# Performance work log

Hardware: AMD Instinct MI355X
Metric: run time of the kernel (lower is better)

## Reference

```python
import jax, jax.numpy as jnp
import numpy as np

DIM = 256
BATCH = 131072


def setup_inputs() -> dict:
    key = jax.random.key(0)
    kx, kl, ku = jax.random.split(key, 3)
    x = jax.random.normal(kx, (BATCH, DIM), dtype=jnp.float32)
    # l: unit lower-triangular (eye + strict lower random), as in __init__
    l = jnp.eye(DIM, dtype=jnp.float32) + jnp.tril(
        jax.random.normal(kl, (DIM, DIM), dtype=jnp.float32), -1)
    # u: unit upper-triangular (eye + strict upper random)
    u = jnp.eye(DIM, dtype=jnp.float32) + jnp.triu(
        jax.random.normal(ku, (DIM, DIM), dtype=jnp.float32), 1)
    # p: fixed random permutation matrix (buffer, not trained)
    perm = np.random.RandomState(0).permutation(DIM)
    p = jnp.zeros((DIM, DIM), dtype=jnp.float32).at[
        np.arange(DIM), perm].set(1.0)
    return {"x": x, "p": p, "l": l, "u": u}


def reference(x, p, l, u):
    # forward (reverse=False): w = p @ l @ u ; y = (w @ x.T).T = x @ w.T
    w = p @ l @ u                      # [dim, dim]
    y = x @ w.T                        # [batch, dim]
    # log|det(w)| = log|det(u)| since p is a permutation (|det|=1) and l is
    # unit-triangular; u is upper-triangular so det(u) = prod(diag(u)).
    log_det = jnp.sum(jnp.log(jnp.abs(jnp.diag(u))))
    return (y, log_det)
```

## Files before the change

### kernel.cpp

```cpp
#include <hip/hip_runtime.h>

#define DIM 256
#define BATCH 131072
#define BM 64

typedef __attribute__((ext_vector_type(8))) short s16x8;
typedef __attribute__((ext_vector_type(8))) unsigned short u16x8;
typedef __attribute__((ext_vector_type(4))) float f32x4;

static __device__ __forceinline__ unsigned short f2bf(float f) {
    unsigned int u = __builtin_bit_cast(unsigned int, f);
    u = (u + 0x7FFFu + ((u >> 16) & 1u)) >> 16;
    return (unsigned short)u;
}

static __device__ __forceinline__ s16x8 cvt8(const float4 a, const float4 b) {
    return (s16x8){ (short)f2bf(a.x), (short)f2bf(a.y), (short)f2bf(a.z), (short)f2bf(a.w),
                    (short)f2bf(b.x), (short)f2bf(b.y), (short)f2bf(b.z), (short)f2bf(b.w) };
}

__global__ void lu_perm(const float* __restrict__ l, const float* __restrict__ u,
                        const float* __restrict__ p, unsigned short* __restrict__ wpk) {
    __shared__ float sL[DIM];
    __shared__ int dest;
    const int i = blockIdx.x, j = threadIdx.x;
    sL[j] = l[i * DIM + j];
    if (p[j * DIM + i] != 0.0f) dest = j;
    __syncthreads();
    float s0 = 0.f, s1 = 0.f, s2 = 0.f, s3 = 0.f;
    #pragma unroll 4
    for (int k = 0; k < DIM; k += 4) {
        s0 = fmaf(sL[k + 0], u[(k + 0) * DIM + j], s0);
        s1 = fmaf(sL[k + 1], u[(k + 1) * DIM + j], s1);
        s2 = fmaf(sL[k + 2], u[(k + 2) * DIM + j], s2);
        s3 = fmaf(sL[k + 3], u[(k + 3) * DIM + j], s3);
    }
    const int d = dest;
    const int idx = ((d >> 4) * 8 + (j >> 5)) * 512 + (((j >> 3) & 3) * 16 + (d & 15)) * 8 + (j & 7);
    wpk[idx] = f2bf((s0 + s1) + (s2 + s3));
}

__global__ void logdet_kernel(const float* __restrict__ u, float* __restrict__ out) {
    const int i = threadIdx.x;
    float v = logf(fabsf(u[i * DIM + i]));
    #pragma unroll
    for (int o = 32; o; o >>= 1) v += __shfl_down(v, o, 64);
    __shared__ float partial[4];
    if ((i & 63) == 0) partial[i >> 6] = v;
    __syncthreads();
    if (i == 0) out[0] = (partial[0] + partial[1]) + (partial[2] + partial[3]);
}

__global__ __launch_bounds__(256, 3) void gemm_xwT(const float* __restrict__ x,
                                                   const unsigned short* __restrict__ wpk,
                                                   float* __restrict__ y) {
    __shared__ unsigned short sA[4 * 8 * 512];

    const int t    = threadIdx.x;
    const int lane = t & 63;
    const int wc   = t >> 6;
    const int lr   = lane & 15;
    const int lg   = lane >> 4;
    const long row0 = (long)blockIdx.x * BM;

    const int sr  = t >> 2;
    const int kq  = t & 3;
    const int r15 = sr & 15;
    const int mb  = t >> 6;
    const float* asrc = x + (row0 + sr) * DIM + kq * 8;
    const int lpx = (kq * 16 + r15) ^ (kq << 1);
    #pragma unroll
    for (int q = 0; q < 8; ++q) {
        const float4 v0 = *(const float4*)(asrc + q * 32);
        const float4 v1 = *(const float4*)(asrc + q * 32 + 4);
        *(s16x8*)&sA[(mb * 8 + q) * 512 + (lpx ^ q) * 8] = cvt8(v0, v1);
    }

    const unsigned short* bbase = wpk + wc * 4 * 8 * 512 + lane * 8;
    const int lx = lane ^ ((lane >> 4) << 1);

    f32x4 acc[4][4];
    #pragma unroll
    for (int mi = 0; mi < 4; mi++)
        #pragma unroll
        for (int n = 0; n < 4; n++) acc[mi][n] = (f32x4){0.f, 0.f, 0.f, 0.f};

    s16x8 bf[2][4];
    #pragma unroll
    for (int n = 0; n < 4; n++)
        bf[0][n] = __builtin_bit_cast(s16x8, *(const u16x8*)(bbase + n * 8 * 512));

    __syncthreads();

    #pragma unroll
    for (int ks = 0; ks < 8; ++ks) {
        if (ks < 7) {
            #pragma unroll
            for (int n = 0; n < 4; n++)
                bf[(ks + 1) & 1][n] = __builtin_bit_cast(s16x8,
                    *(const u16x8*)(bbase + (n * 8 + ks + 1) * 512));
        }
        s16x8 af[4];
        #pragma unroll
        for (int mi = 0; mi < 4; mi++)
            af[mi] = *(const s16x8*)&sA[(mi * 8 + ks) * 512 + (lx ^ ks) * 8];
        #pragma unroll
        for (int mi = 0; mi < 4; mi++)
            #pragma unroll
            for (int n = 0; n < 4; n++)
                acc[mi][n] = __builtin_amdgcn_mfma_f32_16x16x32_bf16(
                    af[mi], bf[ks & 1][n], acc[mi][n], 0, 0, 0);
    }

    __syncthreads();

    float* ep = (float*)sA + wc * 1088;
    #pragma unroll
    for (int mi = 0; mi < 4; ++mi) {
        #pragma unroll
        for (int n = 0; n < 4; n++)
            #pragma unroll
            for (int j = 0; j < 4; j++)
                ep[(lg * 4 + j) * 68 + n * 16 + lr] = acc[mi][n][j];
        #pragma unroll
        for (int it = 0; it < 4; ++it) {
            const int row = it * 4 + lg;
            const float4 v = *(const float4*)&ep[row * 68 + lr * 4];
            *(float4*)&y[(row0 + mi * 16 + row) * DIM + wc * 64 + lr * 4] = v;
        }
    }
}

extern "C" void kernel_launch(void* const* d_in, const int* in_sizes, int n_in,
                              void* d_out, int out_size, void* d_ws, size_t ws_size,
                              hipStream_t stream) {
    const float* x = (const float*)d_in[0];
    const float* p = (const float*)d_in[1];
    const float* l = (const float*)d_in[2];
    const float* u = (const float*)d_in[3];
    float* out = (float*)d_out;

    unsigned short* wpk = (unsigned short*)d_ws;

    lu_perm<<<DIM, DIM, 0, stream>>>(l, u, p, wpk);
    logdet_kernel<<<1, DIM, 0, stream>>>(u, out + (size_t)BATCH * DIM);
    gemm_xwT<<<BATCH / BM, 256, 0, stream>>>(x, wpk, out);
}
```

Measured before the change: 62.94 us.

## Make GEMM persistent over several row tiles with double-buffered x prefetch

The GEMM kernel now uses 512-thread blocks that each walk 8 consecutive 32-row tiles. The next tile's x rows are prefetched into registers while the current tile is converted to bf16 in double-buffered LDS and multiplied. The LDS-staged epilogue is dropped in favour of direct scalar stores of the accumulators, and W fragments are reloaded from global memory for every tile. The intent is to hide global load latency and cut launch and tail overhead. The cost is less coalesced output stores (16 floats per row segment instead of float4) and repeated W reads.

```diff
diff --git a/kernel.cpp b/kernel.cpp
--- a/kernel.cpp
+++ b/kernel.cpp
@@ -2,7 +2,9 @@
 
 #define DIM 256
 #define BATCH 131072
-#define BM 64
+#define BM 32
+#define TPB 8
+#define NBLK (BATCH / (BM * TPB))
 
 typedef __attribute__((ext_vector_type(8))) short s16x8;
 typedef __attribute__((ext_vector_type(8))) unsigned short u16x8;
@@ -51,83 +53,90 @@
     if (i == 0) out[0] = (partial[0] + partial[1]) + (partial[2] + partial[3]);
 }
 
-__global__ __launch_bounds__(256, 3) void gemm_xwT(const float* __restrict__ x,
+__global__ __launch_bounds__(512, 4) void gemm_xwT(const float* __restrict__ x,
                                                    const unsigned short* __restrict__ wpk,
                                                    float* __restrict__ y) {
-    __shared__ unsigned short sA[4 * 8 * 512];
+    __shared__ unsigned short sA[2][16 * 512];
 
     const int t    = threadIdx.x;
     const int lane = t & 63;
-    const int wc   = t >> 6;
+    const int wid  = t >> 6;
     const int lr   = lane & 15;
     const int lg   = lane >> 4;
-    const long row0 = (long)blockIdx.x * BM;
+    const long base = (long)blockIdx.x * (BM * TPB);
 
-    const int sr  = t >> 2;
-    const int kq  = t & 3;
-    const int r15 = sr & 15;
-    const int mb  = t >> 6;
-    const float* asrc = x + (row0 + sr) * DIM + kq * 8;
-    const int lpx = (kq * 16 + r15) ^ (kq << 1);
+    const int srow = t >> 4;
+    const int kq2  = t & 15;
+    const int sks  = kq2 >> 1;
+    const int shs  = kq2 & 1;
+    const int smi  = srow >> 4;
+    const int slr  = srow & 15;
+    const float* asrc = x + (base + srow) * DIM + kq2 * 16;
+
+    const unsigned short* bbase = wpk + (wid * 2) * (8 * 512) + lane * 8;
+
+    float4 pf[2][4];
     #pragma unroll
-    for (int q = 0; q < 8; ++q) {
-        const float4 v0 = *(const float4*)(asrc + q * 32);
-        const float4 v1 = *(const float4*)(asrc + q * 32 + 4);
-        *(s16x8*)&sA[(mb * 8 + q) * 512 + (lpx ^ q) * 8] = cvt8(v0, v1);
-    }
-
-    const unsigned short* bbase = wpk + wc * 4 * 8 * 512 + lane * 8;
-    const int lx = lane ^ ((lane >> 4) << 1);
-
-    f32x4 acc[4][4];
-    #pragma unroll
-    for (int mi = 0; mi < 4; mi++)
-        #pragma unroll
-        for (int n = 0; n < 4; n++) acc[mi][n] = (f32x4){0.f, 0.f, 0.f, 0.f};
-
-    s16x8 bf[2][4];
-    #pragma unroll
-    for (int n = 0; n < 4; n++)
-        bf[0][n] = __builtin_bit_cast(s16x8, *(const u16x8*)(bbase + n * 8 * 512));
-
-    __syncthreads();
+    for (int q = 0; q < 4; q++) pf[0][q] = *(const float4*)(asrc + q * 4);
 
     #pragma unroll
-    for (int ks = 0; ks < 8; ++ks) {
-        if (ks < 7) {
+    for (int tt = 0; tt < TPB; tt++) {
+        const int cur = tt & 1;
+        if (tt + 1 < TPB) {
+            const float* nsrc = asrc + (long)(tt + 1) * BM * DIM;
             #pragma unroll
-            for (int n = 0; n < 4; n++)
-                bf[(ks + 1) & 1][n] = __builtin_bit_cast(s16x8,
-                    *(const u16x8*)(bbase + (n * 8 + ks + 1) * 512));
+            for (int q = 0; q < 4; q++)
+                pf[(tt + 1) & 1][q] = *(const float4*)(nsrc + q * 4);
         }
-        s16x8 af[4];
         #pragma unroll
-        for (int mi = 0; mi < 4; mi++)
-            af[mi] = *(const s16x8*)&sA[(mi * 8 + ks) * 512 + (lx ^ ks) * 8];
+        for (int h = 0; h < 2; h++) {
+            const int lgw = shs * 2 + h;
+            const int lperm = (lgw * 16 + slr) ^ (sks << 1);
+            *(s16x8*)&sA[cur][(sks * 2 + smi) * 512 + lperm * 8] =
+                cvt8(pf[cur][2 * h], pf[cur][2 * h + 1]);
+        }
+        asm volatile("s_waitcnt lgkmcnt(0)" ::: "memory");
+        __builtin_amdgcn_s_barrier();
+
+        f32x4 acc[2][2];
         #pragma unroll
-        for (int mi = 0; mi < 4; mi++)
+        for (int mi = 0; mi < 2; mi++)
             #pragma unroll
-            for (int n = 0; n < 4; n++)
-                acc[mi][n] = __builtin_amdgcn_mfma_f32_16x16x32_bf16(
-                    af[mi], bf[ks & 1][n], acc[mi][n], 0, 0, 0);
-    }
+            for (int n = 0; n < 2; n++) acc[mi][n] = (f32x4){0.f, 0.f, 0.f, 0.f};
 
-    __syncthreads();
+        s16x8 bf[2][2];
+        #pragma unroll
+        for (int n = 0; n < 2; n++)
+            bf[0][n] = __builtin_bit_cast(s16x8, *(const u16x8*)(bbase + (n * 8) * 512));
 
-    float* ep = (float*)sA + wc * 1088;
-    #pragma unroll
-    for (int mi = 0; mi < 4; ++mi) {
         #pragma unroll
-        for (int n = 0; n < 4; n++)
+        for (int ks = 0; ks < 8; ++ks) {
+            if (ks < 7) {
+                #pragma unroll
+                for (int n = 0; n < 2; n++)
+                    bf[(ks + 1) & 1][n] = __builtin_bit_cast(s16x8,
+                        *(const u16x8*)(bbase + (n * 8 + ks + 1) * 512));
+            }
+            s16x8 af[2];
             #pragma unroll
-            for (int j = 0; j < 4; j++)
-                ep[(lg * 4 + j) * 68 + n * 16 + lr] = acc[mi][n][j];
+            for (int mi = 0; mi < 2; mi++)
+                af[mi] = *(const s16x8*)&sA[cur][(ks * 2 + mi) * 512 + (lane ^ (ks << 1)) * 8];
+            #pragma unroll
+            for (int mi = 0; mi < 2; mi++)
+                #pragma unroll
+                for (int n = 0; n < 2; n++)
+                    acc[mi][n] = __builtin_amdgcn_mfma_f32_16x16x32_bf16(
+                        af[mi], bf[ks & 1][n], acc[mi][n], 0, 0, 0);
+        }
+
+        const long r0 = base + (long)tt * BM;
         #pragma unroll
-        for (int it = 0; it < 4; ++it) {
-            const int row = it * 4 + lg;
-            const float4 v = *(const float4*)&ep[row * 68 + lr * 4];
-            *(float4*)&y[(row0 + mi * 16 + row) * DIM + wc * 64 + lr * 4] = v;
-        }
+        for (int mi = 0; mi < 2; mi++)
+            #pragma unroll
+            for (int n = 0; n < 2; n++)
+                #pragma unroll
+                for (int j = 0; j < 4; j++)
+                    y[(r0 + mi * 16 + lg * 4 + j) * DIM + wid * 32 + n * 16 + lr] = acc[mi][n][j];
     }
 }
 
@@ -144,5 +153,5 @@
 
     lu_perm<<<DIM, DIM, 0, stream>>>(l, u, p, wpk);
     logdet_kernel<<<1, DIM, 0, stream>>>(u, out + (size_t)BATCH * DIM);
-    gemm_xwT<<<BATCH / BM, 256, 0, stream>>>(x, wpk, out);
+    gemm_xwT<<<NBLK, 512, 0, stream>>>(x, wpk, out);
 }
```

Measured after the change: 74.34 us. 1.18x slower.
